# Optimization experiments

Hardware: AMD Instinct MI355X
Metric: run time of the kernel (lower is better)

The kernel has to match this reference:

```python
import jax, jax.numpy as jnp
import numpy as np

N_FFT = 512
HOP = N_FFT // 4  # torch.stft default hop_length
TWO_PI = 2.0 * np.pi


def _stft_phase(x):
    """torch.stft(x, n_fft=512, return_complex=True) phase: center reflect-pad,
    rectangular window, onesided rfft. Returns [F, T'] with F = n_fft//2+1."""
    pad = N_FFT // 2
    xp = jnp.pad(x, (pad, pad), mode='reflect')
    n_frames = (xp.shape[0] - N_FFT) // HOP + 1
    idx = (np.arange(n_frames, dtype=np.int32)[:, None] * HOP
           + np.arange(N_FFT, dtype=np.int32)[None, :])
    frames = xp[idx]                      # [T', n_fft]
    spec = jnp.fft.rfft(frames, axis=-1)  # [T', F]
    return jnp.angle(spec).T              # [F, T']


def _anti_wrap(x):
    return jnp.abs(x - jnp.round(x / TWO_PI) * TWO_PI)


def _gd(p):
    # banded matmul with gd_matrix == out[f] = p[f-1] - p[f], out[0] = -p[0]
    return jnp.concatenate([-p[:1], p[:-1] - p[1:]], axis=0)


def _iaf(p):
    # banded matmul with iaf_matrix along time axis
    return jnp.concatenate([-p[:, :1], p[:, :-1] - p[:, 1:]], axis=1)


def setup_inputs() -> dict:
    key = jax.random.key(0)
    k1, k2 = jax.random.split(key)
    T = 4194304  # 2^22 samples (~262 s @ 16 kHz)
    yd = jax.random.normal(k1, (T,), dtype=jnp.float32)
    td = jax.random.normal(k2, (T,), dtype=jnp.float32)
    return {"yd": yd, "td": td}


def reference(yd, td):
    pr = _stft_phase(yd)  # [F, T']
    pg = _stft_phase(td)
    ip_loss = jnp.mean(_anti_wrap(pr - pg))
    gd_loss = jnp.mean(_anti_wrap(_gd(pr) - _gd(pg)))
    iaf_loss = jnp.mean(_anti_wrap(_iaf(pr) - _iaf(pg)))
    return (ip_loss, gd_loss, iaf_loss)
```

## Files before the change

### kernel.cpp

```cpp
#include <hip/hip_runtime.h>
#include <math.h>

#define HOP     128
#define NSLOTS  256
#define FPW     8
#define PI_F    3.14159265358979323846f
#define PI2_F   1.57079632679489661923f
#define K8      0.70710678118654752440f

#define LDS_FENCE() do { __asm__ volatile("" ::: "memory"); \
                         __builtin_amdgcn_wave_barrier(); } while (0)

struct cpx { float x, y; };
__device__ __forceinline__ cpx cadd(cpx a, cpx b){ return {a.x+b.x, a.y+b.y}; }
__device__ __forceinline__ cpx csub(cpx a, cpx b){ return {a.x-b.x, a.y-b.y}; }
__device__ __forceinline__ cpx cmul(cpx a, cpx b){
    return {fmaf(a.x,b.x,-a.y*b.y), fmaf(a.x,b.y, a.y*b.x)};
}
__device__ __forceinline__ cpx cmulc(cpx a, cpx b){
    return {fmaf(a.x,b.x, a.y*b.y), fmaf(a.y,b.x,-a.x*b.y)};
}

__device__ __forceinline__ float abs_angle(float re, float im) {
    float a = fabsf(im), b = fabsf(re);
    float mn = fminf(a, b), mx = fmaxf(a, b);
    float t = __fdividef(mn, fmaxf(mx, 1e-37f));
    float t2 = t * t;
    float p = fmaf(t2, -0.0117212f, 0.05265332f);
    p = fmaf(t2, p, -0.11643287f);
    p = fmaf(t2, p, 0.19354346f);
    p = fmaf(t2, p, -0.33262347f);
    p = fmaf(t2, p, 0.99997726f);
    float r = t * p;
    r = (a > b) ? (PI2_F - r) : r;
    r = (re < 0.f) ? (PI_F - r) : r;
    return r;
}

__device__ __forceinline__ void dft8(cpx v[8]) {
    cpx a0=cadd(v[0],v[4]), a1=cadd(v[1],v[5]), a2=cadd(v[2],v[6]), a3=cadd(v[3],v[7]);
    cpx b0=csub(v[0],v[4]), b1=csub(v[1],v[5]), b2=csub(v[2],v[6]), b3=csub(v[3],v[7]);
    b1 = cpx{K8*(b1.x+b1.y), K8*(b1.y-b1.x)};
    b2 = cpx{b2.y, -b2.x};
    b3 = cpx{K8*(b3.y-b3.x), -K8*(b3.x+b3.y)};
    cpx c0=cadd(a0,a2), c2=csub(a0,a2);
    cpx c1=cadd(a1,a3), c3=csub(a1,a3); c3 = cpx{c3.y, -c3.x};
    cpx d0=cadd(b0,b2), d2=csub(b0,b2);
    cpx d1=cadd(b1,b3), d3=csub(b1,b3); d3 = cpx{d3.y, -d3.x};
    v[0]=cadd(c0,c1); v[4]=csub(c0,c1);
    v[2]=cadd(c2,c3); v[6]=csub(c2,c3);
    v[1]=cadd(d0,d1); v[5]=csub(d0,d1);
    v[3]=cadd(d2,d3); v[7]=csub(d2,d3);
}

__global__ __launch_bounds__(256, 4) void phase_loss_kernel(
        const float* __restrict__ y, const float* __restrict__ g,
        float* __restrict__ acc, int* __restrict__ ticket,
        float* __restrict__ out, int T, int n_frames, float inv_count) {
    __shared__ float2 xch_all[4][576];
    __shared__ float2 cl_all[4][258];
    __shared__ float wsum[3][4];
    __shared__ int is_last;

    const int tid  = threadIdx.x;
    const int lane = tid & 63;
    const int wid  = tid >> 6;
    float2* xch = xch_all[wid];
    float2* Cl  = cl_all[wid] + 1;

    cpx tw1[8], tw2[8];
    #pragma unroll
    for (int k = 0; k < 8; ++k) {
        float a1 = -(2.0f * PI_F / 512.0f) * (float)(lane * k);
        __sincosf(a1, &tw1[k].y, &tw1[k].x);
        float a2 = -(2.0f * PI_F / 64.0f) * (float)((lane & 7) * k);
        __sincosf(a2, &tw2[k].y, &tw2[k].x);
    }

    float ip = 0.f, gd = 0.f, iaf = 0.f;
    cpx Cp[5];
    const int tmax_int = (T - 256) / HOP;

    auto do_frame = [&](int t, bool accum, bool hp) {
        cpx v[8];
        const int base = t * HOP - 256 + lane;
        if (t >= 2 && t <= tmax_int) {
            #pragma unroll
            for (int r = 0; r < 8; ++r) {
                int j = base + r * 64;
                v[r].x = y[j]; v[r].y = g[j];
            }
        } else {
            #pragma unroll
            for (int r = 0; r < 8; ++r) {
                int j = base + r * 64;
                j = (j < 0) ? -j : j;
                j = (j >= T) ? (2 * T - 2 - j) : j;
                v[r].x = y[j]; v[r].y = g[j];
            }
        }
        dft8(v);
        #pragma unroll
        for (int k = 1; k < 8; ++k) v[k] = cmul(v[k], tw1[k]);
        LDS_FENCE();
        #pragma unroll
        for (int k = 0; k < 8; ++k)
            xch[k * 72 + lane] = make_float2(v[k].x, v[k].y);
        LDS_FENCE();
        {
            const int ra = (lane >> 3) * 72 + (lane & 7);
            #pragma unroll
            for (int r = 0; r < 8; ++r) {
                float2 tmp = xch[ra + r * 8];
                v[r] = cpx{tmp.x, tmp.y};
            }
        }
        dft8(v);
        #pragma unroll
        for (int k = 1; k < 8; ++k) v[k] = cmul(v[k], tw2[k]);
        LDS_FENCE();
        #pragma unroll
        for (int k = 0; k < 8; ++k)
            xch[k * 65 + lane] = make_float2(v[k].x, v[k].y);
        LDS_FENCE();
        {
            const int ra = (lane >> 3) * 65 + (lane & 7) * 8;
            #pragma unroll
            for (int r = 0; r < 8; ++r) {
                float2 tmp = xch[ra + r];
                v[r] = cpx{tmp.x, tmp.y};
            }
        }
        dft8(v);
        float2* Z = xch;
        LDS_FENCE();
        #pragma unroll
        for (int j = 0; j < 8; ++j)
            Z[lane + (j << 6)] = make_float2(v[j].x, v[j].y);
        LDS_FENCE();
        cpx Cc[5];
        #pragma unroll
        for (int jj = 0; jj < 5; ++jj) {
            const int f = lane + (jj << 6);
            float2 tmp = Z[(512 - f) & 511];
            float ur = v[jj].x + tmp.x, ui = v[jj].y - tmp.y;
            float vx = v[jj].x - tmp.x, vy = v[jj].y + tmp.y;
            Cc[jj].x = fmaf(ur, vy, -ui * vx);
            Cc[jj].y = fmaf(ur, vx,  ui * vy);
        }
        if (accum) {
            LDS_FENCE();
            #pragma unroll
            for (int jj = 0; jj < 4; ++jj)
                Cl[lane + (jj << 6)] = make_float2(Cc[jj].x, Cc[jj].y);
            if (lane == 0) Cl[256] = make_float2(Cc[4].x, Cc[4].y);
            LDS_FENCE();
            cpx cm[4];
            #pragma unroll
            for (int jj = 0; jj < 4; ++jj) {
                float2 tmp = Cl[lane + (jj << 6) - 1];
                cm[jj] = cpx{tmp.x, tmp.y};
            }
            float2 c255 = Cl[255];
            #pragma unroll
            for (int jj = 0; jj < 4; ++jj) {
                cpx cc = Cc[jj];
                float aw = abs_angle(cc.x, cc.y);
                ip += aw;
                cpx qg = cmulc(cm[jj], cc);
                float gt = abs_angle(qg.x, qg.y);
                gd += (jj == 0 && lane == 0) ? aw : gt;
                if (hp) {
                    cpx qi = cmulc(Cp[jj], cc);
                    iaf += abs_angle(qi.x, qi.y);
                } else {
                    iaf += aw;
                }
            }
            if (lane == 0) {
                cpx cc = Cc[4];
                float aw = abs_angle(cc.x, cc.y);
                ip += aw;
                cpx qg = cmulc(cpx{c255.x, c255.y}, cc);
                gd += abs_angle(qg.x, qg.y);
                if (hp) {
                    cpx qi = cmulc(Cp[4], cc);
                    iaf += abs_angle(qi.x, qi.y);
                } else {
                    iaf += aw;
                }
            }
        }
        #pragma unroll
        for (int jj = 0; jj < 5; ++jj) Cp[jj] = Cc[jj];
    };

    const int chain   = (blockIdx.x << 2) | wid;
    const int nchains = (int)(gridDim.x << 2);
    const int t0 = chain * FPW;
    int tend = t0 + FPW;
    if (chain == nchains - 1) tend = n_frames;
    const bool havep = (t0 > 0);

    if (havep) do_frame(t0 - 1, false, false);
    #pragma unroll 2
    for (int t = t0; t < tend; ++t)
        do_frame(t, true, havep || (t > t0));

    __syncthreads();
    for (int off = 32; off; off >>= 1) {
        ip  += __shfl_down(ip, off);
        gd  += __shfl_down(gd, off);
        iaf += __shfl_down(iaf, off);
    }
    if (lane == 0) { wsum[0][wid] = ip; wsum[1][wid] = gd; wsum[2][wid] = iaf; }
    __syncthreads();
    if (tid == 0) {
        const int slot = (int)(blockIdx.x & (NSLOTS - 1));
        atomicAdd(acc + 0 * NSLOTS + slot, wsum[0][0] + wsum[0][1] + wsum[0][2] + wsum[0][3]);
        atomicAdd(acc + 1 * NSLOTS + slot, wsum[1][0] + wsum[1][1] + wsum[1][2] + wsum[1][3]);
        atomicAdd(acc + 2 * NSLOTS + slot, wsum[2][0] + wsum[2][1] + wsum[2][2] + wsum[2][3]);
        __threadfence();
        is_last = (atomicAdd(ticket, 1) == (int)gridDim.x - 1);
    }
    __syncthreads();
    if (is_last) {
        for (int l = 0; l < 3; l++) {
            float vv = __hip_atomic_load(acc + l * NSLOTS + tid,
                                         __ATOMIC_RELAXED, __HIP_MEMORY_SCOPE_AGENT);
            for (int off = 32; off; off >>= 1) vv += __shfl_down(vv, off);
            if (lane == 0) wsum[l][wid] = vv;
        }
        __syncthreads();
        if (tid < 3)
            out[tid] = (wsum[tid][0] + wsum[tid][1] + wsum[tid][2] + wsum[tid][3]) * inv_count;
    }
}

extern "C" void kernel_launch(void* const* d_in, const int* in_sizes, int n_in,
                              void* d_out, int out_size, void* d_ws, size_t ws_size,
                              hipStream_t stream) {
    const float* y = (const float*)d_in[0];
    const float* g = (const float*)d_in[1];
    float* out = (float*)d_out;
    float* acc = (float*)d_ws;
    int* ticket = (int*)((char*)d_ws + 3 * NSLOTS * sizeof(float));
    const int T = in_sizes[0];
    const int n_frames = T / HOP + 1;
    int n_blocks = n_frames / (FPW * 4);
    if (n_blocks < 1) n_blocks = 1;

    hipMemsetAsync(d_ws, 0, 3 * NSLOTS * sizeof(float) + sizeof(int), stream);
    const float inv_count = 1.0f / (257.0f * (float)n_frames);
    phase_loss_kernel<<<n_blocks, 256, 0, stream>>>(y, g, acc, ticket, out,
                                                    T, n_frames, inv_count);
}
```

Baseline: 134.6 us.

## Halve frames per wave, raise occupancy, XOR-swizzle LDS, shuffle neighbor bins

Frames per wave chain drop from 8 to 4, and launch bounds now request 8 blocks per SM, which spreads work over more waves and raises occupancy. The padded LDS exchange buffers are replaced by unpadded 512-entry buffers that use XOR-swizzled indices to avoid bank conflicts. The per-wave Cl LDS array and its store/load round trip, used to fetch the f-1 neighbour bin for the group-delay term, is replaced by wave shuffles. The shorter chains repeat the warm-up (overlap) frame more often, which adds redundant FFT work, and the higher occupancy target may force register spills.

```diff
diff --git a/kernel.cpp b/kernel.cpp
--- a/kernel.cpp
+++ b/kernel.cpp
@@ -3,7 +3,7 @@
 
 #define HOP     128
 #define NSLOTS  256
-#define FPW     8
+#define FPW     4
 #define PI_F    3.14159265358979323846f
 #define PI2_F   1.57079632679489661923f
 #define K8      0.70710678118654752440f
@@ -53,12 +53,11 @@
     v[3]=cadd(d2,d3); v[7]=csub(d2,d3);
 }
 
-__global__ __launch_bounds__(256, 4) void phase_loss_kernel(
+__global__ __launch_bounds__(256, 8) void phase_loss_kernel(
         const float* __restrict__ y, const float* __restrict__ g,
         float* __restrict__ acc, int* __restrict__ ticket,
         float* __restrict__ out, int T, int n_frames, float inv_count) {
-    __shared__ float2 xch_all[4][576];
-    __shared__ float2 cl_all[4][258];
+    __shared__ float2 xch_all[4][512];
     __shared__ float wsum[3][4];
     __shared__ int is_last;
 
@@ -66,7 +65,6 @@
     const int lane = tid & 63;
     const int wid  = tid >> 6;
     float2* xch = xch_all[wid];
-    float2* Cl  = cl_all[wid] + 1;
 
     cpx tw1[8], tw2[8];
     #pragma unroll
@@ -80,6 +78,9 @@
     float ip = 0.f, gd = 0.f, iaf = 0.f;
     cpx Cp[5];
     const int tmax_int = (T - 256) / HOP;
+    const int ra1 = (lane >> 3) * 72 + (lane & 7);
+    const int ra2 = (lane >> 3) * 65 + (lane & 7) * 8;
+    const int rsl = (lane + 63) & 63;
 
     auto do_frame = [&](int t, bool accum, bool hp) {
         cpx v[8];
@@ -105,15 +106,12 @@
         LDS_FENCE();
         #pragma unroll
         for (int k = 0; k < 8; ++k)
-            xch[k * 72 + lane] = make_float2(v[k].x, v[k].y);
-        LDS_FENCE();
-        {
-            const int ra = (lane >> 3) * 72 + (lane & 7);
-            #pragma unroll
-            for (int r = 0; r < 8; ++r) {
-                float2 tmp = xch[ra + r * 8];
-                v[r] = cpx{tmp.x, tmp.y};
-            }
+            xch[lane ^ (72 * k)] = make_float2(v[k].x, v[k].y);
+        LDS_FENCE();
+        #pragma unroll
+        for (int r = 0; r < 8; ++r) {
+            float2 tmp = xch[ra1 ^ (r << 3)];
+            v[r] = cpx{tmp.x, tmp.y};
         }
         dft8(v);
         #pragma unroll
@@ -121,15 +119,12 @@
         LDS_FENCE();
         #pragma unroll
         for (int k = 0; k < 8; ++k)
-            xch[k * 65 + lane] = make_float2(v[k].x, v[k].y);
-        LDS_FENCE();
-        {
-            const int ra = (lane >> 3) * 65 + (lane & 7) * 8;
-            #pragma unroll
-            for (int r = 0; r < 8; ++r) {
-                float2 tmp = xch[ra + r];
-                v[r] = cpx{tmp.x, tmp.y};
-            }
+            xch[lane ^ (65 * k)] = make_float2(v[k].x, v[k].y);
+        LDS_FENCE();
+        #pragma unroll
+        for (int r = 0; r < 8; ++r) {
+            float2 tmp = xch[ra2 ^ r];
+            v[r] = cpx{tmp.x, tmp.y};
         }
         dft8(v);
         float2* Z = xch;
@@ -149,25 +144,17 @@
             Cc[jj].y = fmaf(ur, vx,  ui * vy);
         }
         if (accum) {
-            LDS_FENCE();
-            #pragma unroll
-            for (int jj = 0; jj < 4; ++jj)
-                Cl[lane + (jj << 6)] = make_float2(Cc[jj].x, Cc[jj].y);
-            if (lane == 0) Cl[256] = make_float2(Cc[4].x, Cc[4].y);
-            LDS_FENCE();
-            cpx cm[4];
+            cpx rprev = {0.f, 0.f};
             #pragma unroll
             for (int jj = 0; jj < 4; ++jj) {
-                float2 tmp = Cl[lane + (jj << 6) - 1];
-                cm[jj] = cpx{tmp.x, tmp.y};
-            }
-            float2 c255 = Cl[255];
-            #pragma unroll
-            for (int jj = 0; jj < 4; ++jj) {
+                cpx rj;
+                rj.x = __shfl(Cc[jj].x, rsl, 64);
+                rj.y = __shfl(Cc[jj].y, rsl, 64);
+                cpx cmj = (jj > 0 && lane == 0) ? rprev : rj;
                 cpx cc = Cc[jj];
                 float aw = abs_angle(cc.x, cc.y);
                 ip += aw;
-                cpx qg = cmulc(cm[jj], cc);
+                cpx qg = cmulc(cmj, cc);
                 float gt = abs_angle(qg.x, qg.y);
                 gd += (jj == 0 && lane == 0) ? aw : gt;
                 if (hp) {
@@ -176,12 +163,13 @@
                 } else {
                     iaf += aw;
                 }
+                rprev = rj;
             }
             if (lane == 0) {
                 cpx cc = Cc[4];
                 float aw = abs_angle(cc.x, cc.y);
                 ip += aw;
-                cpx qg = cmulc(cpx{c255.x, c255.y}, cc);
+                cpx qg = cmulc(rprev, cc);
                 gd += abs_angle(qg.x, qg.y);
                 if (hp) {
                     cpx qi = cmulc(Cp[4], cc);
```

Result: slower. 377.7 us (+180.7%).
